# Optimization experiments

Hardware: AMD Instinct MI355X
Metric: run time of the kernel (lower is better)

The kernel has to match this reference:

```python
import jax, jax.numpy as jnp
import numpy as np

EPS = 1e-05

def setup_inputs() -> dict:
    key = jax.random.key(0)
    N, U = 131072, 256  # n_features (total nodes), n_units
    x = jax.random.normal(key, (N, U), dtype=jnp.float32)
    gamma = jnp.ones((N, U), dtype=jnp.float32)
    beta = jnp.ones((N, U), dtype=jnp.float32)
    return {"x": x, "gamma": gamma, "beta": beta, "batch_size": 64}

def reference(x, gamma, beta, batch_size):
    N, U = x.shape
    n = N // batch_size  # nodes per graph (tf.split into equal chunks)
    xr = x.reshape(batch_size, n, U)
    mean = jnp.mean(xr, axis=1, keepdims=True)            # per-graph, per-unit mean
    std = jnp.std(xr, axis=1, keepdims=True)              # population std (ddof=0), as tf.reduce_std
    xn = ((xr - mean) / (std + EPS)).reshape(N, U)
    return gamma * xn + beta
```

## Files before the change

### kernel.cpp

```cpp
#include <hip/hip_runtime.h>

#define GN_EPS 1e-5f

constexpr int U      = 256;
constexpr int NPG    = 2048;
constexpr int NGRAPH = 64;
constexpr int UPB    = 32;
constexpr int GPB    = UPB / 4;
constexpr int NSLICE = U / UPB;
constexpr int BLK    = 512;
constexpr int ROWS   = BLK / GPB;
constexpr int ITERS  = NPG / ROWS;

__global__ __launch_bounds__(BLK) void graphnorm_kernel(
    const float* __restrict__ x,
    const float* __restrict__ gamma,
    const float* __restrict__ beta,
    float* __restrict__ out)
{
    const int slice = blockIdx.x & (NSLICE - 1);
    const int graph = blockIdx.x / NSLICE;
    const int t     = threadIdx.x;
    const int grp   = t & (GPB - 1);
    const int r0    = t >> 3;
    const int col   = slice * UPB + grp * 4;
    const size_t base = (size_t)graph * NPG * U + (size_t)col;

    float4 s = make_float4(0.f, 0.f, 0.f, 0.f);
    float4 q = make_float4(0.f, 0.f, 0.f, 0.f);
#pragma unroll 8
    for (int i = 0; i < ITERS; ++i) {
        const int row = r0 + i * ROWS;
        const float4 v = *reinterpret_cast<const float4*>(x + base + (size_t)row * U);
        s.x += v.x; s.y += v.y; s.z += v.z; s.w += v.w;
        q.x += v.x * v.x; q.y += v.y * v.y; q.z += v.z * v.z; q.w += v.w * v.w;
    }

#pragma unroll
    for (int m = 8; m <= 32; m <<= 1) {
        s.x += __shfl_xor(s.x, m); s.y += __shfl_xor(s.y, m);
        s.z += __shfl_xor(s.z, m); s.w += __shfl_xor(s.w, m);
        q.x += __shfl_xor(q.x, m); q.y += __shfl_xor(q.y, m);
        q.z += __shfl_xor(q.z, m); q.w += __shfl_xor(q.w, m);
    }

    __shared__ float4 ssum[BLK / 64][GPB];
    __shared__ float4 ssq [BLK / 64][GPB];
    __shared__ float4 smean[GPB];
    __shared__ float4 sinv [GPB];

    const int wave = t >> 6;
    const int lane = t & 63;
    if (lane < GPB) {
        ssum[wave][lane] = s;
        ssq [wave][lane] = q;
    }
    __syncthreads();

    if (t < 64) {
        const int g = t & 7;
        const int w = t >> 3;
        float4 s2 = ssum[w][g];
        float4 q2 = ssq [w][g];
#pragma unroll
        for (int m = 8; m <= 32; m <<= 1) {
            s2.x += __shfl_xor(s2.x, m); s2.y += __shfl_xor(s2.y, m);
            s2.z += __shfl_xor(s2.z, m); s2.w += __shfl_xor(s2.w, m);
            q2.x += __shfl_xor(q2.x, m); q2.y += __shfl_xor(q2.y, m);
            q2.z += __shfl_xor(q2.z, m); q2.w += __shfl_xor(q2.w, m);
        }
        if (t < GPB) {
            const float invn = 1.0f / (float)NPG;
            float4 mean, inv;
            mean.x = s2.x * invn; mean.y = s2.y * invn;
            mean.z = s2.z * invn; mean.w = s2.w * invn;
            float vx = fmaxf(q2.x * invn - mean.x * mean.x, 0.f);
            float vy = fmaxf(q2.y * invn - mean.y * mean.y, 0.f);
            float vz = fmaxf(q2.z * invn - mean.z * mean.z, 0.f);
            float vw = fmaxf(q2.w * invn - mean.w * mean.w, 0.f);
            inv.x = 1.0f / (sqrtf(vx) + GN_EPS);
            inv.y = 1.0f / (sqrtf(vy) + GN_EPS);
            inv.z = 1.0f / (sqrtf(vz) + GN_EPS);
            inv.w = 1.0f / (sqrtf(vw) + GN_EPS);
            smean[t] = mean;
            sinv [t] = inv;
        }
    }
    __syncthreads();

    const float4 mean = smean[grp];
    const float4 inv  = sinv [grp];

#pragma unroll 4
    for (int i = 0; i < ITERS; ++i) {
        const int row = r0 + i * ROWS;
        const size_t off = base + (size_t)row * U;
        const float4 v  = *reinterpret_cast<const float4*>(x + off);
        const float4 g4 = *reinterpret_cast<const float4*>(gamma + off);
        const float4 b4 = *reinterpret_cast<const float4*>(beta + off);
        float4 o;
        o.x = fmaf(g4.x, (v.x - mean.x) * inv.x, b4.x);
        o.y = fmaf(g4.y, (v.y - mean.y) * inv.y, b4.y);
        o.z = fmaf(g4.z, (v.z - mean.z) * inv.z, b4.z);
        o.w = fmaf(g4.w, (v.w - mean.w) * inv.w, b4.w);
        *reinterpret_cast<float4*>(out + off) = o;
    }
}

extern "C" void kernel_launch(void* const* d_in, const int* in_sizes, int n_in,
                              void* d_out, int out_size, void* d_ws, size_t ws_size,
                              hipStream_t stream) {
    const float* x     = (const float*)d_in[0];
    const float* gamma = (const float*)d_in[1];
    const float* beta  = (const float*)d_in[2];
    float* out = (float*)d_out;
    (void)in_sizes; (void)n_in; (void)out_size; (void)d_ws; (void)ws_size;

    const int grid = NGRAPH * NSLICE;
    graphnorm_kernel<<<grid, BLK, 0, stream>>>(x, gamma, beta, out);
}
```

Measured before the change: 439.8 us.

## Split graph norm into partial-stats, finalize, and normalize kernels

```diff
diff --git a/kernel.cpp b/kernel.cpp
--- a/kernel.cpp
+++ b/kernel.cpp
@@ -2,108 +2,131 @@
 
 #define GN_EPS 1e-5f
 
-constexpr int U      = 256;
-constexpr int NPG    = 2048;
-constexpr int NGRAPH = 64;
-constexpr int UPB    = 32;
-constexpr int GPB    = UPB / 4;
-constexpr int NSLICE = U / UPB;
-constexpr int BLK    = 512;
-constexpr int ROWS   = BLK / GPB;
-constexpr int ITERS  = NPG / ROWS;
+constexpr int U       = 256;
+constexpr int NPG     = 2048;
+constexpr int NGRAPH  = 64;
+constexpr int UF4     = U / 4;
 
-__global__ __launch_bounds__(BLK) void graphnorm_kernel(
-    const float* __restrict__ x,
-    const float* __restrict__ gamma,
-    const float* __restrict__ beta,
-    float* __restrict__ out)
+constexpr int CH      = 16;
+constexpr int RPC     = NPG / CH;
+constexpr int K1_BLK  = 256;
+constexpr int K1_WAVES = K1_BLK / 64;
+constexpr int K1_ITERS = RPC / K1_WAVES;
+
+constexpr int CH3     = 32;
+constexpr int RPC3    = NPG / CH3;
+constexpr int K3_BLK  = 256;
+constexpr int K3_ITERS = (RPC3 * UF4) / K3_BLK;
+
+constexpr size_t WS_SUM_OFF  = 0;
+constexpr size_t WS_SQ_OFF   = (size_t)NGRAPH * CH * U;
+constexpr size_t WS_MEAN_OFF = WS_SQ_OFF + (size_t)NGRAPH * CH * U;
+constexpr size_t WS_INV_OFF  = WS_MEAN_OFF + (size_t)NGRAPH * U;
+
+__global__ __launch_bounds__(K1_BLK) void gn_partial(
+    const float* __restrict__ x, float* __restrict__ ws)
 {
-    const int slice = blockIdx.x & (NSLICE - 1);
-    const int graph = blockIdx.x / NSLICE;
+    const int chunk = blockIdx.x & (CH - 1);
+    const int graph = blockIdx.x / CH;
     const int t     = threadIdx.x;
-    const int grp   = t & (GPB - 1);
-    const int r0    = t >> 3;
-    const int col   = slice * UPB + grp * 4;
-    const size_t base = (size_t)graph * NPG * U + (size_t)col;
+    const int wave  = t >> 6;
+    const int lane  = t & 63;
+
+    const size_t row0 = (size_t)graph * NPG + (size_t)chunk * RPC + wave;
+    const float4* xr = reinterpret_cast<const float4*>(x) + row0 * UF4 + lane;
 
     float4 s = make_float4(0.f, 0.f, 0.f, 0.f);
     float4 q = make_float4(0.f, 0.f, 0.f, 0.f);
 #pragma unroll 8
-    for (int i = 0; i < ITERS; ++i) {
-        const int row = r0 + i * ROWS;
-        const float4 v = *reinterpret_cast<const float4*>(x + base + (size_t)row * U);
+    for (int i = 0; i < K1_ITERS; ++i) {
+        const float4 v = xr[(size_t)i * K1_WAVES * UF4];
         s.x += v.x; s.y += v.y; s.z += v.z; s.w += v.w;
         q.x += v.x * v.x; q.y += v.y * v.y; q.z += v.z * v.z; q.w += v.w * v.w;
     }
 
+    __shared__ float4 ssum[K1_WAVES][64];
+    __shared__ float4 ssq [K1_WAVES][64];
+    ssum[wave][lane] = s;
+    ssq [wave][lane] = q;
+    __syncthreads();
+
+    if (t < 64) {
+        float4 s2 = ssum[0][t];
+        float4 q2 = ssq [0][t];
 #pragma unroll
-    for (int m = 8; m <= 32; m <<= 1) {
-        s.x += __shfl_xor(s.x, m); s.y += __shfl_xor(s.y, m);
-        s.z += __shfl_xor(s.z, m); s.w += __shfl_xor(s.w, m);
-        q.x += __shfl_xor(q.x, m); q.y += __shfl_xor(q.y, m);
-        q.z += __shfl_xor(q.z, m); q.w += __shfl_xor(q.w, m);
+        for (int w = 1; w < K1_WAVES; ++w) {
+            const float4 a = ssum[w][t];
+            const float4 b = ssq [w][t];
+            s2.x += a.x; s2.y += a.y; s2.z += a.z; s2.w += a.w;
+            q2.x += b.x; q2.y += b.y; q2.z += b.z; q2.w += b.w;
+        }
+        const size_t o = ((size_t)graph * CH + chunk) * UF4 + t;
+        reinterpret_cast<float4*>(ws + WS_SUM_OFF)[o] = s2;
+        reinterpret_cast<float4*>(ws + WS_SQ_OFF )[o] = q2;
     }
+}
 
-    __shared__ float4 ssum[BLK / 64][GPB];
-    __shared__ float4 ssq [BLK / 64][GPB];
-    __shared__ float4 smean[GPB];
-    __shared__ float4 sinv [GPB];
+__global__ __launch_bounds__(U) void gn_finalize(float* __restrict__ ws)
+{
+    const int graph = blockIdx.x;
+    const int t     = threadIdx.x;
 
-    const int wave = t >> 6;
-    const int lane = t & 63;
-    if (lane < GPB) {
-        ssum[wave][lane] = s;
-        ssq [wave][lane] = q;
+    const float* psum = ws + WS_SUM_OFF + (size_t)graph * CH * U + t;
+    const float* psq  = ws + WS_SQ_OFF  + (size_t)graph * CH * U + t;
+    float s = 0.f, q = 0.f;
+#pragma unroll
+    for (int c = 0; c < CH; ++c) {
+        s += psum[(size_t)c * U];
+        q += psq [(size_t)c * U];
+    }
+    const float invn = 1.0f / (float)NPG;
+    const float mean = s * invn;
+    const float var  = fmaxf(q * invn - mean * mean, 0.f);
+    ws[WS_MEAN_OFF + (size_t)graph * U + t] = mean;
+    ws[WS_INV_OFF  + (size_t)graph * U + t] = 1.0f / (sqrtf(var) + GN_EPS);
+}
+
+__global__ __launch_bounds__(K3_BLK) void gn_normalize(
+    const float* __restrict__ x,
+    const float* __restrict__ gamma,
+    const float* __restrict__ beta,
+    const float* __restrict__ ws,
+    float* __restrict__ out)
+{
+    const int chunk = blockIdx.x & (CH3 - 1);
+    const int graph = blockIdx.x / CH3;
+    const int t     = threadIdx.x;
+
+    __shared__ float4 smean[UF4];
+    __shared__ float4 sinv [UF4];
+    if (t < UF4) {
+        smean[t] = reinterpret_cast<const float4*>(ws + WS_MEAN_OFF + (size_t)graph * U)[t];
+        sinv [t] = reinterpret_cast<const float4*>(ws + WS_INV_OFF  + (size_t)graph * U)[t];
     }
     __syncthreads();
 
-    if (t < 64) {
-        const int g = t & 7;
-        const int w = t >> 3;
-        float4 s2 = ssum[w][g];
-        float4 q2 = ssq [w][g];
-#pragma unroll
-        for (int m = 8; m <= 32; m <<= 1) {
-            s2.x += __shfl_xor(s2.x, m); s2.y += __shfl_xor(s2.y, m);
-            s2.z += __shfl_xor(s2.z, m); s2.w += __shfl_xor(s2.w, m);
-            q2.x += __shfl_xor(q2.x, m); q2.y += __shfl_xor(q2.y, m);
-            q2.z += __shfl_xor(q2.z, m); q2.w += __shfl_xor(q2.w, m);
-        }
-        if (t < GPB) {
-            const float invn = 1.0f / (float)NPG;
-            float4 mean, inv;
-            mean.x = s2.x * invn; mean.y = s2.y * invn;
-            mean.z = s2.z * invn; mean.w = s2.w * invn;
-            float vx = fmaxf(q2.x * invn - mean.x * mean.x, 0.f);
-            float vy = fmaxf(q2.y * invn - mean.y * mean.y, 0.f);
-            float vz = fmaxf(q2.z * invn - mean.z * mean.z, 0.f);
-            float vw = fmaxf(q2.w * invn - mean.w * mean.w, 0.f);
-            inv.x = 1.0f / (sqrtf(vx) + GN_EPS);
-            inv.y = 1.0f / (sqrtf(vy) + GN_EPS);
-            inv.z = 1.0f / (sqrtf(vz) + GN_EPS);
-            inv.w = 1.0f / (sqrtf(vw) + GN_EPS);
-            smean[t] = mean;
-            sinv [t] = inv;
-        }
-    }
-    __syncthreads();
-
-    const float4 mean = smean[grp];
-    const float4 inv  = sinv [grp];
+    const size_t row0 = (size_t)graph * NPG + (size_t)chunk * RPC3;
+    const size_t f4base = row0 * UF4;
+    const float4* xv = reinterpret_cast<const float4*>(x)     + f4base;
+    const float4* gv = reinterpret_cast<const float4*>(gamma) + f4base;
+    const float4* bv = reinterpret_cast<const float4*>(beta)  + f4base;
+    float4*       ov = reinterpret_cast<float4*>(out)         + f4base;
 
 #pragma unroll 4
-    for (int i = 0; i < ITERS; ++i) {
-        const int row = r0 + i * ROWS;
-        const size_t off = base + (size_t)row * U;
-        const float4 v  = *reinterpret_cast<const float4*>(x + off);
-        const float4 g4 = *reinterpret_cast<const float4*>(gamma + off);
-        const float4 b4 = *reinterpret_cast<const float4*>(beta + off);
+    for (int i = 0; i < K3_ITERS; ++i) {
+        const int idx = i * K3_BLK + t;
+        const int f4  = idx & (UF4 - 1);
+        const float4 v  = xv[idx];
+        const float4 g4 = gv[idx];
+        const float4 b4 = bv[idx];
+        const float4 m  = smean[f4];
+        const float4 iv = sinv [f4];
         float4 o;
-        o.x = fmaf(g4.x, (v.x - mean.x) * inv.x, b4.x);
-        o.y = fmaf(g4.y, (v.y - mean.y) * inv.y, b4.y);
-        o.z = fmaf(g4.z, (v.z - mean.z) * inv.z, b4.z);
-        o.w = fmaf(g4.w, (v.w - mean.w) * inv.w, b4.w);
-        *reinterpret_cast<float4*>(out + off) = o;
+        o.x = fmaf(g4.x, (v.x - m.x) * iv.x, b4.x);
+        o.y = fmaf(g4.y, (v.y - m.y) * iv.y, b4.y);
+        o.z = fmaf(g4.z, (v.z - m.z) * iv.z, b4.z);
+        o.w = fmaf(g4.w, (v.w - m.w) * iv.w, b4.w);
+        ov[idx] = o;
     }
 }
 
@@ -114,8 +137,10 @@
     const float* gamma = (const float*)d_in[1];
     const float* beta  = (const float*)d_in[2];
     float* out = (float*)d_out;
-    (void)in_sizes; (void)n_in; (void)out_size; (void)d_ws; (void)ws_size;
+    float* ws  = (float*)d_ws;
+    (void)in_sizes; (void)n_in; (void)out_size; (void)ws_size;
 
-    const int grid = NGRAPH * NSLICE;
-    graphnorm_kernel<<<grid, BLK, 0, stream>>>(x, gamma, beta, out);
+    gn_partial <<<NGRAPH * CH,  K1_BLK, 0, stream>>>(x, ws);
+    gn_finalize<<<NGRAPH,       U,      0, stream>>>(ws);
+    gn_normalize<<<NGRAPH * CH3, K3_BLK, 0, stream>>>(x, gamma, beta, ws, out);
 }
```

Result: faster. 414.9 us (-5.7%).
